# Performance work log

Hardware: AMD Instinct MI355X
Metric: run time of the kernel (lower is better)

The kernel has to match this reference:

```python
import jax, jax.numpy as jnp
import numpy as np

N_NODES = 50000
N_EDGES = 200000
H = 128
L = 6
NODE_IN = 9
EDGE_IN = 10
OUT = 3


def _glorot(key, shape):
    fan_in = shape[0]
    return jax.random.normal(key, shape, dtype=jnp.float32) * (1.0 / np.sqrt(fan_in))


def setup_inputs() -> dict:
    key = jax.random.key(0)
    ks = jax.random.split(key, 32)
    x = jax.random.normal(ks[0], (N_NODES, NODE_IN), dtype=jnp.float32)
    edge_attr = jax.random.normal(ks[1], (N_EDGES, EDGE_IN), dtype=jnp.float32)
    edge_index = jax.random.randint(ks[2], (2, N_EDGES), 0, N_NODES, dtype=jnp.int32)
    bc_disp = (jax.random.uniform(ks[3], (N_NODES, 2)) < 0.05).astype(jnp.float32)
    bc_rot = (jax.random.uniform(ks[4], (N_NODES, 1)) < 0.05).astype(jnp.float32)
    inp = {
        'x': x, 'edge_attr': edge_attr, 'edge_index': edge_index,
        'bc_disp': bc_disp, 'bc_rot': bc_rot,
        # node encoder MLP(NODE_IN,[H],H)
        'enc_n_W1': _glorot(ks[5], (NODE_IN, H)), 'enc_n_b1': jnp.zeros((H,), jnp.float32),
        'enc_n_W2': _glorot(ks[6], (H, H)), 'enc_n_b2': jnp.zeros((H,), jnp.float32),
        # edge encoder MLP(EDGE_IN,[H],H)
        'enc_e_W1': _glorot(ks[7], (EDGE_IN, H)), 'enc_e_b1': jnp.zeros((H,), jnp.float32),
        'enc_e_W2': _glorot(ks[8], (H, H)), 'enc_e_b2': jnp.zeros((H,), jnp.float32),
        # L message-passing layers: msg MLP(3H->H->H), update MLP(2H->H->H), stacked on dim 0
        'mp_msg_W1': jnp.stack([_glorot(jax.random.fold_in(ks[9], i), (3 * H, H)) for i in range(L)]),
        'mp_msg_b1': jnp.zeros((L, H), jnp.float32),
        'mp_msg_W2': jnp.stack([_glorot(jax.random.fold_in(ks[10], i), (H, H)) for i in range(L)]),
        'mp_msg_b2': jnp.zeros((L, H), jnp.float32),
        'mp_upd_W1': jnp.stack([_glorot(jax.random.fold_in(ks[11], i), (2 * H, H)) for i in range(L)]),
        'mp_upd_b1': jnp.zeros((L, H), jnp.float32),
        'mp_upd_W2': jnp.stack([_glorot(jax.random.fold_in(ks[12], i), (H, H)) for i in range(L)]),
        'mp_upd_b2': jnp.zeros((L, H), jnp.float32),
        # decoder MLP(H,[H,64],OUT)
        'dec_W1': _glorot(ks[13], (H, H)), 'dec_b1': jnp.zeros((H,), jnp.float32),
        'dec_W2': _glorot(ks[14], (H, 64)), 'dec_b2': jnp.zeros((64,), jnp.float32),
        'dec_W3': _glorot(ks[15], (64, OUT)), 'dec_b3': jnp.zeros((OUT,), jnp.float32),
    }
    return inp


def _pignn_forward(x, edge_attr, edge_index, bc_disp, bc_rot,
                   enc_n_W1, enc_n_b1, enc_n_W2, enc_n_b2,
                   enc_e_W1, enc_e_b1, enc_e_W2, enc_e_b2,
                   mp_msg_W1, mp_msg_b1, mp_msg_W2, mp_msg_b2,
                   mp_upd_W1, mp_upd_b1, mp_upd_W2, mp_upd_b2,
                   dec_W1, dec_b1, dec_W2, dec_b2, dec_W3, dec_b3):
    relu = jax.nn.relu
    n = x.shape[0]
    src, dst = edge_index[0], edge_index[1]

    # encoders: Linear -> ReLU -> Linear
    h = relu(x @ enc_n_W1 + enc_n_b1) @ enc_n_W2 + enc_n_b2            # [N, H]
    e = relu(edge_attr @ enc_e_W1 + enc_e_b1) @ enc_e_W2 + enc_e_b2    # [E, H]

    def mp_step(h, params):
        mW1, mb1, mW2, mb2, uW1, ub1, uW2, ub2 = params
        m_in = jnp.concatenate([h[src], h[dst], e], axis=-1)           # [E, 3H]
        m = relu(m_in @ mW1 + mb1) @ mW2 + mb2                         # [E, H]
        agg = jax.ops.segment_sum(m, dst, num_segments=n)              # [N, H]
        u_in = jnp.concatenate([h, agg], axis=-1)                      # [N, 2H]
        upd = relu(u_in @ uW1 + ub1) @ uW2 + ub2                       # [N, H]
        return h + upd, None                                           # residual

    h, _ = jax.lax.scan(mp_step, h,
                        (mp_msg_W1, mp_msg_b1, mp_msg_W2, mp_msg_b2,
                         mp_upd_W1, mp_upd_b1, mp_upd_W2, mp_upd_b2))

    # decoder: H -> H -> 64 -> OUT with ReLU between layers
    d = relu(h @ dec_W1 + dec_b1)
    d = relu(d @ dec_W2 + dec_b2)
    pred = d @ dec_W3 + dec_b3                                         # [N, 3]

    # hard boundary conditions
    disp_mask = 1.0 - bc_disp
    rot_mask = 1.0 - bc_rot
    return jnp.concatenate([pred[:, 0:2] * disp_mask, pred[:, 2:3] * rot_mask], axis=1)


def reference(x, edge_attr, edge_index, bc_disp, bc_rot,
              enc_n_W1, enc_n_b1, enc_n_W2, enc_n_b2,
              enc_e_W1, enc_e_b1, enc_e_W2, enc_e_b2,
              mp_msg_W1, mp_msg_b1, mp_msg_W2, mp_msg_b2,
              mp_upd_W1, mp_upd_b1, mp_upd_W2, mp_upd_b2,
              dec_W1, dec_b1, dec_W2, dec_b2, dec_W3, dec_b3):
    return _pignn_forward(x, edge_attr, edge_index, bc_disp, bc_rot,
                          enc_n_W1, enc_n_b1, enc_n_W2, enc_n_b2,
                          enc_e_W1, enc_e_b1, enc_e_W2, enc_e_b2,
                          mp_msg_W1, mp_msg_b1, mp_msg_W2, mp_msg_b2,
                          mp_upd_W1, mp_upd_b1, mp_upd_W2, mp_upd_b2,
                          dec_W1, dec_b1, dec_W2, dec_b2, dec_W3, dec_b3)
```

## Files before the change

### kernel.cpp

```cpp
#include <hip/hip_runtime.h>

#define NN 50000
#define NE 200000
#define HD 128

typedef unsigned short us4 __attribute__((ext_vector_type(4)));
typedef unsigned short us8 __attribute__((ext_vector_type(8)));
typedef short s8 __attribute__((ext_vector_type(8)));
typedef float f4 __attribute__((ext_vector_type(4)));

#define SA 136
#define SA32 40
#define SC2 68

__device__ __forceinline__ float b2f(unsigned short u) {
    union { unsigned i; float f; } v; v.i = ((unsigned)u) << 16; return v.f;
}
__device__ __forceinline__ unsigned short f2b(float x) {
    union { float f; unsigned i; } v; v.f = x;
    unsigned r = v.i + 0x7fffu + ((v.i >> 16) & 1u);
    return (unsigned short)(r >> 16);
}
struct hl2 { short hi, lo; };
__device__ __forceinline__ hl2 split2(float x) {
    unsigned short h = f2b(x);
    hl2 r;
    r.hi = (short)h;
    r.lo = (short)f2b(x - b2f(h));
    return r;
}

__global__ __launch_bounds__(256) void zeroi_k(int* __restrict__ p, int n) {
    int i = blockIdx.x * 256 + threadIdx.x;
    if (i < n) p[i] = 0;
}
__global__ __launch_bounds__(256) void zerof_k(float* __restrict__ p, long n) {
    long i = (long)blockIdx.x * 256 + threadIdx.x;
    if (i < n) p[i] = 0.f;
}

__global__ __launch_bounds__(256) void hist_k(const int* __restrict__ dst, int* __restrict__ cnt) {
    int i = blockIdx.x * 256 + threadIdx.x;
    if (i < NE) atomicAdd(&cnt[dst[i]], 1);
}
__global__ __launch_bounds__(256) void scan1_k(const int* __restrict__ cnt, int* __restrict__ bsum) {
    __shared__ int sc[256];
    int i = blockIdx.x * 256 + threadIdx.x;
    sc[threadIdx.x] = (i < NN) ? cnt[i] : 0;
    __syncthreads();
    for (int off = 128; off > 0; off >>= 1) {
        if (threadIdx.x < off) sc[threadIdx.x] += sc[threadIdx.x + off];
        __syncthreads();
    }
    if (threadIdx.x == 0) bsum[blockIdx.x] = sc[0];
}
__global__ __launch_bounds__(256) void scan2_k(int* __restrict__ bsum, int nb) {
    __shared__ int sc[256];
    int t = threadIdx.x;
    int v = (t < nb) ? bsum[t] : 0;
    sc[t] = v;
    __syncthreads();
    for (int off = 1; off < 256; off <<= 1) {
        int a = (t >= off) ? sc[t - off] : 0;
        __syncthreads();
        sc[t] += a;
        __syncthreads();
    }
    if (t < nb) bsum[t] = sc[t] - v;
}
__global__ __launch_bounds__(256) void scan3_k(const int* __restrict__ cnt, const int* __restrict__ bsum,
                                               int* __restrict__ rp, float* __restrict__ deg) {
    __shared__ int sc[256];
    int t = threadIdx.x;
    int i = blockIdx.x * 256 + t;
    int v = (i < NN) ? cnt[i] : 0;
    sc[t] = v;
    __syncthreads();
    for (int off = 1; off < 256; off <<= 1) {
        int a = (t >= off) ? sc[t - off] : 0;
        __syncthreads();
        sc[t] += a;
        __syncthreads();
    }
    int incl = sc[t];
    if (i < NN) {
        rp[i] = bsum[blockIdx.x] + incl - v;
        deg[i] = (float)v;
        if (i == NN - 1) rp[NN] = bsum[blockIdx.x] + incl;
    }
}
__global__ __launch_bounds__(256) void posbuild_k(const int* __restrict__ src, const int* __restrict__ dst,
                                                  const int* __restrict__ rp, int* __restrict__ cur,
                                                  int* __restrict__ pos, int* __restrict__ srcS,
                                                  int* __restrict__ dstS) {
    int i = blockIdx.x * 256 + threadIdx.x;
    if (i >= NE) return;
    int d = dst[i];
    int p = rp[d] + atomicAdd(&cur[d], 1);
    pos[i] = p;
    srcS[p] = src[i];
    dstS[p] = d;
}

__global__ __launch_bounds__(256) void mini_k(const float* __restrict__ W2m, const float* __restrict__ uW1b,
                                              const float* __restrict__ b2m,
                                              float* __restrict__ W2u, float* __restrict__ b2u) {
    int r = blockIdx.x * 16 + (threadIdx.x >> 4);
    int c0 = (threadIdx.x & 15) * 8;
    float a[8] = {};
    for (int k = 0; k < HD; ++k) {
        float w = W2m[r * HD + k];
        const float* u = uW1b + k * HD + c0;
        float4 u0 = *(const float4*)u, u1 = *(const float4*)(u + 4);
        a[0] = fmaf(w, u0.x, a[0]); a[1] = fmaf(w, u0.y, a[1]);
        a[2] = fmaf(w, u0.z, a[2]); a[3] = fmaf(w, u0.w, a[3]);
        a[4] = fmaf(w, u1.x, a[4]); a[5] = fmaf(w, u1.y, a[5]);
        a[6] = fmaf(w, u1.z, a[6]); a[7] = fmaf(w, u1.w, a[7]);
    }
    *(float4*)(W2u + r * HD + c0)     = float4{a[0], a[1], a[2], a[3]};
    *(float4*)(W2u + r * HD + c0 + 4) = float4{a[4], a[5], a[6], a[7]};
    if (blockIdx.x == 0 && threadIdx.x < 16) {
        int cc = threadIdx.x * 8;
        float b[8] = {};
        for (int k = 0; k < HD; ++k) {
            float w = b2m[k];
            const float* u = uW1b + k * HD + cc;
            float4 u0 = *(const float4*)u, u1 = *(const float4*)(u + 4);
            b[0] = fmaf(w, u0.x, b[0]); b[1] = fmaf(w, u0.y, b[1]);
            b[2] = fmaf(w, u0.z, b[2]); b[3] = fmaf(w, u0.w, b[3]);
            b[4] = fmaf(w, u1.x, b[4]); b[5] = fmaf(w, u1.y, b[5]);
            b[6] = fmaf(w, u1.z, b[6]); b[7] = fmaf(w, u1.w, b[7]);
        }
        *(float4*)(b2u + cc)     = float4{b[0], b[1], b[2], b[3]};
        *(float4*)(b2u + cc + 4) = float4{b[4], b[5], b[6], b[7]};
    }
}
__global__ __launch_bounds__(256) void wtL_k(const float* __restrict__ msgW1, const float* __restrict__ updW1,
                                             const float* __restrict__ updW2, const float* __restrict__ W2uF,
                                             unsigned short* __restrict__ dst) {
    int idx = blockIdx.x * 256 + threadIdx.x;
    int m = idx >> 14;
    int r = idx & 16383;
    int n = r >> 7, k = r & 127;
    float v;
    switch (m) {
        case 0: v = msgW1[(long)k * HD + n]; break;
        case 1: v = msgW1[(long)(128 + k) * HD + n]; break;
        case 2: v = msgW1[(long)(256 + k) * HD + n]; break;
        case 3: v = updW1[(long)k * HD + n]; break;
        case 4: v = updW2[(long)k * HD + n]; break;
        default: v = W2uF[(long)k * HD + n]; break;
    }
    hl2 p = split2(v);
    dst[(long)m * 32768 + n * HD + k] = (unsigned short)p.hi;
    dst[(long)m * 32768 + 16384 + n * HD + k] = (unsigned short)p.lo;
}
__global__ __launch_bounds__(256) void wtE_k(const float* __restrict__ nW1, const float* __restrict__ nW2,
                                             const float* __restrict__ eW1, const float* __restrict__ eW2,
                                             unsigned short* __restrict__ dst) {
    int idx = blockIdx.x * 256 + threadIdx.x;
    float v; long off; int pos, sz;
    if (idx < 4096) {
        int n = idx >> 5, k = idx & 31;
        v = (k < 9) ? nW1[k * HD + n] : 0.f; off = 0; pos = idx; sz = 4096;
    } else if (idx < 20480) {
        int r = idx - 4096; int n = r >> 7, k = r & 127;
        v = nW2[k * HD + n]; off = 8192; pos = r; sz = 16384;
    } else if (idx < 24576) {
        int r = idx - 20480; int n = r >> 5, k = r & 31;
        v = (k < 10) ? eW1[k * HD + n] : 0.f; off = 40960; pos = r; sz = 4096;
    } else {
        int r = idx - 24576; int n = r >> 7, k = r & 127;
        v = eW2[k * HD + n]; off = 49152; pos = r; sz = 16384;
    }
    hl2 p = split2(v);
    dst[off + pos] = (unsigned short)p.hi;
    dst[off + sz + pos] = (unsigned short)p.lo;
}

__device__ __forceinline__ void stageA_f32_split(short* __restrict__ At, short* __restrict__ Al,
                                                 const float* __restrict__ A, int bm, int M, int tid) {
#pragma unroll
    for (int t = 0; t < 4; ++t) {
        int c = tid + t * 256;
        int row = c >> 4, k8 = (c & 15) * 8;
        int gr = bm + row;
        s8 vh = (s8)0, vl = (s8)0;
        if (gr < M) {
            const float* p = A + (long)gr * HD + k8;
            f4 a = *(const f4*)p, b = *(const f4*)(p + 4);
#pragma unroll
            for (int i = 0; i < 4; ++i) {
                hl2 pa = split2(a[i]);
                hl2 pb = split2(b[i]);
                vh[i] = pa.hi; vl[i] = pa.lo;
                vh[4 + i] = pb.hi; vl[4 + i] = pb.lo;
            }
        }
        *(s8*)(At + row * SA + k8) = vh;
        *(s8*)(Al + row * SA + k8) = vl;
    }
}
__device__ __forceinline__ void stageA_b16(short* __restrict__ At, const unsigned short* __restrict__ A,
                                           int bm, int M, int tid) {
#pragma unroll
    for (int t = 0; t < 4; ++t) {
        int c = tid + t * 256;
        int row = c >> 4, k8 = (c & 15) * 8;
        int gr = bm + row;
        s8 v = (s8)0;
        if (gr < M) v = *(const s8*)(A + (long)gr * HD + k8);
        *(s8*)(At + row * SA + k8) = v;
    }
}
__device__ __forceinline__ void stage_segsum_split(short* __restrict__ At, short* __restrict__ Al,
                                                   const unsigned short* __restrict__ Pe,
                                                   const int* __restrict__ rowp,
                                                   int bm, int M, int tid) {
#pragma unroll
    for (int t = 0; t < 4; ++t) {
        int c = tid + t * 256;
        int row = c >> 4, k8 = (c & 15) * 8;
        int gr = bm + row;
        float sum[8] = {};
        if (gr < M) {
            int e0 = rowp[gr], e1 = rowp[gr + 1];
            for (int e = e0; e < e1; ++e) {
                us8 v = *(const us8*)(Pe + (long)e * HD + k8);
#pragma unroll
                for (int i = 0; i < 8; ++i) sum[i] += b2f(v[i]);
            }
        }
        s8 vh, vl;
#pragma unroll
        for (int i = 0; i < 8; ++i) {
            hl2 p = split2(sum[i]);
            vh[i] = p.hi; vl[i] = p.lo;
        }
        *(s8*)(At + row * SA + k8) = vh;
        *(s8*)(Al + row * SA + k8) = vl;
    }
}
__device__ __forceinline__ void loadB2(s8 b[2][4], const unsigned short* __restrict__ W,
                                       int sw, int nk, int w, int lane) {
    const int r16 = lane & 15, q8 = (lane >> 4) * 8;
#pragma unroll
    for (int ct = 0; ct < 2; ++ct)
#pragma unroll 4
        for (int ks = 0; ks < nk; ++ks)
            b[ct][ks] = *(const s8*)((const short*)W + (long)((2 * w + ct) * 16 + r16) * sw + ks * 32 + q8);
}
__device__ __forceinline__ void mfma3_reg(f4 acc[4][2], const short* __restrict__ At,
                                          const short* __restrict__ Al, int sa,
                                          const s8 bh[2][4], const s8 bl[2][4], int nk, int lane) {
    const int r16 = lane & 15, q8 = (lane >> 4) * 8;
#pragma unroll 4
    for (int ks = 0; ks < nk; ++ks)
#pragma unroll
        for (int rt = 0; rt < 4; ++rt) {
            s8 ah = *(const s8*)(At + (rt * 16 + r16) * sa + ks * 32 + q8);
            s8 al = *(const s8*)(Al + (rt * 16 + r16) * sa + ks * 32 + q8);
#pragma unroll
            for (int ct = 0; ct < 2; ++ct) {
                acc[rt][ct] = __builtin_amdgcn_mfma_f32_16x16x32_bf16(ah, bh[ct][ks], acc[rt][ct], 0, 0, 0);
                acc[rt][ct] = __builtin_amdgcn_mfma_f32_16x16x32_bf16(al, bh[ct][ks], acc[rt][ct], 0, 0, 0);
                acc[rt][ct] = __builtin_amdgcn_mfma_f32_16x16x32_bf16(ah, bl[ct][ks], acc[rt][ct], 0, 0, 0);
            }
        }
}
__device__ __forceinline__ void mfmaE_reg(f4 acc[4][2], const short* __restrict__ At, int sa,
                                          const s8 bh[2][4], const s8 bl[2][4], int nk, int lane) {
    const int r16 = lane & 15, q8 = (lane >> 4) * 8;
#pragma unroll 4
    for (int ks = 0; ks < nk; ++ks)
#pragma unroll
        for (int rt = 0; rt < 4; ++rt) {
            s8 a = *(const s8*)(At + (rt * 16 + r16) * sa + ks * 32 + q8);
#pragma unroll
            for (int ct = 0; ct < 2; ++ct) {
                acc[rt][ct] = __builtin_amdgcn_mfma_f32_16x16x32_bf16(a, bh[ct][ks], acc[rt][ct], 0, 0, 0);
                acc[rt][ct] = __builtin_amdgcn_mfma_f32_16x16x32_bf16(a, bl[ct][ks], acc[rt][ct], 0, 0, 0);
            }
        }
}
__device__ __forceinline__ void dumpC_half2(float* __restrict__ Cd, const f4 acc[4][2],
                                            int half, int w, int lane) {
    if ((w >> 1) != half) return;
    const int col0 = lane & 15, rq = (lane >> 4) * 4;
    const int bc = (w & 1) * 2;
#pragma unroll
    for (int rt = 0; rt < 4; ++rt)
#pragma unroll
        for (int ct = 0; ct < 2; ++ct)
#pragma unroll
            for (int r = 0; r < 4; ++r)
                Cd[(rt * 16 + rq + r) * SC2 + (bc + ct) * 16 + col0] = acc[rt][ct][r];
}
#define ACC_ZERO2(acc) { f4 z_ = {0.f, 0.f, 0.f, 0.f}; \
    for (int r_ = 0; r_ < 4; ++r_) for (int c_ = 0; c_ < 2; ++c_) acc[r_][c_] = z_; }

__global__ __launch_bounds__(256) void dual_k(const float* __restrict__ h,
                                              const unsigned short* __restrict__ W1aT,
                                              const unsigned short* __restrict__ W1bT,
                                              unsigned short* __restrict__ Hs, unsigned short* __restrict__ Hd,
                                              int M) {
    __shared__ __align__(16) short At[64 * SA];
    __shared__ __align__(16) short Al[64 * SA];
    __shared__ __align__(16) float Cd[64 * SC2];
    const int tid = threadIdx.x, lane = tid & 63, w = tid >> 6, tx = tid & 15, ty = tid >> 4;
    const int bm = blockIdx.x * 64;
    s8 bh[2][4], bl[2][4];
    loadB2(bh, W1aT, HD, 4, w, lane);
    loadB2(bl, W1aT + 16384, HD, 4, w, lane);
    stageA_f32_split(At, Al, h, bm, M, tid);
    __syncthreads();
    f4 acc[4][2]; ACC_ZERO2(acc);
    mfma3_reg(acc, At, Al, SA, bh, bl, 4, lane);
    loadB2(bh, W1bT, HD, 4, w, lane);
    loadB2(bl, W1bT + 16384, HD, 4, w, lane);
#pragma unroll
    for (int half = 0; half < 2; ++half) {
        __syncthreads();
        dumpC_half2(Cd, acc, half, w, lane);
        __syncthreads();
        int c4 = half * 64 + tx * 4;
#pragma unroll
        for (int i = 0; i < 4; ++i) {
            int row = ty * 4 + i, gr = bm + row;
            if (gr >= M) continue;
            f4 v = *(const f4*)(Cd + row * SC2 + tx * 4);
            us4 o;
#pragma unroll
            for (int j = 0; j < 4; ++j) o[j] = f2b(v[j]);
            *(us4*)(Hs + (long)gr * HD + c4) = o;
        }
    }
    ACC_ZERO2(acc);
    mfma3_reg(acc, At, Al, SA, bh, bl, 4, lane);
#pragma unroll
    for (int half = 0; half < 2; ++half) {
        __syncthreads();
        dumpC_half2(Cd, acc, half, w, lane);
        __syncthreads();
        int c4 = half * 64 + tx * 4;
#pragma unroll
        for (int i = 0; i < 4; ++i) {
            int row = ty * 4 + i, gr = bm + row;
            if (gr >= M) continue;
            f4 v = *(const f4*)(Cd + row * SC2 + tx * 4);
            us4 o;
#pragma unroll
            for (int j = 0; j < 4; ++j) o[j] = f2b(v[j]);
            *(us4*)(Hd + (long)gr * HD + c4) = o;
        }
    }
}

__global__ __launch_bounds__(256) void edge_k(const unsigned short* __restrict__ eS,
                                              const unsigned short* __restrict__ Hs,
                                              const unsigned short* __restrict__ Hd,
                                              const int* __restrict__ srcS, const int* __restrict__ dstS,
                                              const unsigned short* __restrict__ W1cT,
                                              const float* __restrict__ b1,
                                              unsigned short* __restrict__ Pe) {
    __shared__ __align__(16) short At[64 * SA];
    __shared__ __align__(16) float Cd[64 * SC2];
    const int tid = threadIdx.x, lane = tid & 63, w = tid >> 6, tx = tid & 15, ty = tid >> 4;
    const int bm = blockIdx.x * 64;
    s8 bh[2][4], bl[2][4];
    loadB2(bh, W1cT, HD, 4, w, lane);
    loadB2(bl, W1cT + 16384, HD, 4, w, lane);
    stageA_b16(At, eS, bm, NE, tid);
    __syncthreads();
    f4 acc[4][2]; ACC_ZERO2(acc);
    mfmaE_reg(acc, At, SA, bh, bl, 4, lane);
#pragma unroll
    for (int half = 0; half < 2; ++half) {
        __syncthreads();
        dumpC_half2(Cd, acc, half, w, lane);
        __syncthreads();
        int c4 = half * 64 + tx * 4;
        f4 bv = *(const f4*)(b1 + c4);
#pragma unroll
        for (int i = 0; i < 4; ++i) {
            int row = ty * 4 + i, edge = bm + row;
            int s = srcS[edge], d = dstS[edge];
            us4 hs = *(const us4*)(Hs + (long)s * HD + c4);
            us4 hd = *(const us4*)(Hd + (long)d * HD + c4);
            f4 cv = *(const f4*)(Cd + row * SC2 + tx * 4);
            us4 o;
#pragma unroll
            for (int j = 0; j < 4; ++j)
                o[j] = f2b(fmaxf(cv[j] + bv[j] + b2f(hs[j]) + b2f(hd[j]), 0.f));
            *(us4*)(Pe + (long)edge * HD + c4) = o;
        }
    }
}

__global__ __launch_bounds__(256) void upd_k(float* __restrict__ h,
                                             const unsigned short* __restrict__ Pe,
                                             const int* __restrict__ rowp,
                                             const unsigned short* __restrict__ uW1aT,
                                             const unsigned short* __restrict__ W2uT,
                                             const float* __restrict__ ub1, const float* __restrict__ b2u,
                                             const float* __restrict__ deg,
                                             const unsigned short* __restrict__ uW2T,
                                             const float* __restrict__ ub2, int M) {
    __shared__ __align__(16) short At[64 * SA];
    __shared__ __align__(16) short Al[64 * SA];
    __shared__ __align__(16) float Cd[64 * SC2];
    const int tid = threadIdx.x, lane = tid & 63, w = tid >> 6, tx = tid & 15, ty = tid >> 4;
    const int bm = blockIdx.x * 64;
    s8 bh[2][4], bl[2][4];
    f4 acc[4][2]; ACC_ZERO2(acc);
    loadB2(bh, uW1aT, HD, 4, w, lane);
    loadB2(bl, uW1aT + 16384, HD, 4, w, lane);
    stageA_f32_split(At, Al, h, bm, M, tid);
    __syncthreads();
    mfma3_reg(acc, At, Al, SA, bh, bl, 4, lane);
    loadB2(bh, W2uT, HD, 4, w, lane);
    loadB2(bl, W2uT + 16384, HD, 4, w, lane);
    __syncthreads();
    stage_segsum_split(At, Al, Pe, rowp, bm, M, tid);
    __syncthreads();
    mfma3_reg(acc, At, Al, SA, bh, bl, 4, lane);
    loadB2(bh, uW2T, HD, 4, w, lane);
    loadB2(bl, uW2T + 16384, HD, 4, w, lane);
    __syncthreads();
    {
        const int col0 = lane & 15, rq = (lane >> 4) * 4;
        float u1[2], u2[2];
#pragma unroll
        for (int ct = 0; ct < 2; ++ct) {
            int col = (2 * w + ct) * 16 + col0;
            u1[ct] = ub1[col]; u2[ct] = b2u[col];
        }
        float dgv[16];
#pragma unroll
        for (int rt = 0; rt < 4; ++rt)
#pragma unroll
            for (int r = 0; r < 4; ++r) {
                int gr = bm + rt * 16 + rq + r;
                dgv[rt * 4 + r] = (gr < M) ? deg[gr] : 0.f;
            }
#pragma unroll
        for (int rt = 0; rt < 4; ++rt)
#pragma unroll
            for (int ct = 0; ct < 2; ++ct)
#pragma unroll
                for (int r = 0; r < 4; ++r) {
                    float p = fmaxf(acc[rt][ct][r] + u1[ct] + dgv[rt * 4 + r] * u2[ct], 0.f);
                    hl2 pp = split2(p);
                    int off = (rt * 16 + rq + r) * SA + (2 * w + ct) * 16 + col0;
                    At[off] = pp.hi;
                    Al[off] = pp.lo;
                }
    }
    __syncthreads();
    ACC_ZERO2(acc);
    mfma3_reg(acc, At, Al, SA, bh, bl, 4, lane);
#pragma unroll
    for (int half = 0; half < 2; ++half) {
        __syncthreads();
        dumpC_half2(Cd, acc, half, w, lane);
        __syncthreads();
        int c4 = half * 64 + tx * 4;
        f4 u0 = *(const f4*)(ub2 + c4);
#pragma unroll
        for (int i = 0; i < 4; ++i) {
            int row = ty * 4 + i, gr = bm + row;
            if (gr >= M) continue;
            float* hp = h + (long)gr * HD + c4;
            f4 a = *(f4*)hp;
            f4 cv = *(const f4*)(Cd + row * SC2 + tx * 4);
#pragma unroll
            for (int j = 0; j < 4; ++j) a[j] += cv[j] + u0[j];
            *(f4*)hp = a;
        }
    }
}

template<bool SCAT>
__global__ __launch_bounds__(256) void enc_k(const float* __restrict__ A, int KIN,
                                             const unsigned short* __restrict__ W1T, const float* __restrict__ b1,
                                             const unsigned short* __restrict__ W2T, const float* __restrict__ b2,
                                             float* __restrict__ outF, unsigned short* __restrict__ outB,
                                             const int* __restrict__ pos, int M) {
    __shared__ __align__(16) short At[64 * SA];
    __shared__ __align__(16) short Al[64 * SA];
    __shared__ __align__(16) float Cd[64 * SC2];
    const int tid = threadIdx.x, lane = tid & 63, w = tid >> 6, tx = tid & 15, ty = tid >> 4;
    const int bm = blockIdx.x * 64;
    s8 bh[2][4], bl[2][4];
    loadB2(bh, W1T, 32, 1, w, lane);
    loadB2(bl, W1T + 4096, 32, 1, w, lane);
    {
        int row = tid >> 2, k8 = (tid & 3) * 8;
        int gr = bm + row;
        s8 vh = (s8)0, vl = (s8)0;
        if (gr < M) {
#pragma unroll
            for (int i = 0; i < 8; ++i) {
                int k = k8 + i;
                if (k < KIN) {
                    hl2 p = split2(A[(long)gr * KIN + k]);
                    vh[i] = p.hi; vl[i] = p.lo;
                }
            }
        }
        *(s8*)(At + row * SA32 + k8) = vh;
        *(s8*)(Al + row * SA32 + k8) = vl;
    }
    __syncthreads();
    f4 acc[4][2]; ACC_ZERO2(acc);
    mfma3_reg(acc, At, Al, SA32, bh, bl, 1, lane);
    loadB2(bh, W2T, HD, 4, w, lane);
    loadB2(bl, W2T + 16384, HD, 4, w, lane);
    __syncthreads();
    {
        const int col0 = lane & 15, rq = (lane >> 4) * 4;
        float bb[2];
#pragma unroll
        for (int ct = 0; ct < 2; ++ct) bb[ct] = b1[(2 * w + ct) * 16 + col0];
#pragma unroll
        for (int rt = 0; rt < 4; ++rt)
#pragma unroll
            for (int ct = 0; ct < 2; ++ct)
#pragma unroll
                for (int r = 0; r < 4; ++r) {
                    float p = fmaxf(acc[rt][ct][r] + bb[ct], 0.f);
                    hl2 pp = split2(p);
                    int off = (rt * 16 + rq + r) * SA + (2 * w + ct) * 16 + col0;
                    At[off] = pp.hi;
                    Al[off] = pp.lo;
                }
    }
    __syncthreads();
    ACC_ZERO2(acc);
    mfma3_reg(acc, At, Al, SA, bh, bl, 4, lane);
#pragma unroll
    for (int half = 0; half < 2; ++half) {
        __syncthreads();
        dumpC_half2(Cd, acc, half, w, lane);
        __syncthreads();
        int c4 = half * 64 + tx * 4;
        f4 bv = *(const f4*)(b2 + c4);
#pragma unroll
        for (int i = 0; i < 4; ++i) {
            int row = ty * 4 + i, gr = bm + row;
            if (gr >= M) continue;
            f4 cv = *(const f4*)(Cd + row * SC2 + tx * 4);
            if constexpr (SCAT) {
                int p = pos[gr];
                us4 o;
#pragma unroll
                for (int j = 0; j < 4; ++j) o[j] = f2b(cv[j] + bv[j]);
                *(us4*)(outB + (long)p * HD + c4) = o;
            } else {
                f4 o;
#pragma unroll
                for (int j = 0; j < 4; ++j) o[j] = cv[j] + bv[j];
                *(f4*)(outF + (long)gr * HD + c4) = o;
            }
        }
    }
}

__global__ __launch_bounds__(256) void dec_k(
    const float* __restrict__ h,
    const float* __restrict__ W1, const float* __restrict__ b1,
    const float* __restrict__ W2, const float* __restrict__ b2,
    const float* __restrict__ W3, const float* __restrict__ b3,
    const float* __restrict__ bc_disp, const float* __restrict__ bc_rot,
    float* __restrict__ outp, int M)
{
    __shared__ float As[64][33];
    __shared__ float Ws[32][HD];
    __shared__ float P[64][HD + 1];
    __shared__ float D2[64][65];
    const int tid = threadIdx.x, tx = tid & 15, ty = tid >> 4;
    const int bm = blockIdx.x * 64;
    float acc[4][8] = {};

    for (int kk = 0; kk < HD; kk += 32) {
        int r = tid >> 2, cc0 = (tid & 3) * 8, gr = bm + r;
#pragma unroll
        for (int i = 0; i < 8; ++i)
            As[r][cc0 + i] = (gr < M) ? h[(long)gr * HD + kk + cc0 + i] : 0.f;
        int k = tid >> 3, n0 = (tid & 7) * 16;
#pragma unroll
        for (int i = 0; i < 16; ++i)
            Ws[k][n0 + i] = W1[(kk + k) * HD + n0 + i];
        __syncthreads();
#pragma unroll
        for (int k2 = 0; k2 < 32; ++k2) {
            float a0 = As[ty * 4 + 0][k2], a1 = As[ty * 4 + 1][k2];
            float a2 = As[ty * 4 + 2][k2], a3 = As[ty * 4 + 3][k2];
#pragma unroll
            for (int j = 0; j < 8; ++j) {
                float ww = Ws[k2][tx * 8 + j];
                acc[0][j] = fmaf(a0, ww, acc[0][j]);
                acc[1][j] = fmaf(a1, ww, acc[1][j]);
                acc[2][j] = fmaf(a2, ww, acc[2][j]);
                acc[3][j] = fmaf(a3, ww, acc[3][j]);
            }
        }
        __syncthreads();
    }
#pragma unroll
    for (int i = 0; i < 4; ++i) {
        int row = ty * 4 + i;
#pragma unroll
        for (int j = 0; j < 8; ++j) {
            int col = tx * 8 + j;
            P[row][col] = fmaxf(acc[i][j] + b1[col], 0.f);
        }
    }
    __syncthreads();
    float acc2[4][4] = {};
    for (int kk = 0; kk < HD; kk += 32) {
        int idx = tid * 8;
        int k = idx >> 6, n0 = idx & 63;
#pragma unroll
        for (int i = 0; i < 8; ++i)
            Ws[k][n0 + i] = W2[(kk + k) * 64 + n0 + i];
        __syncthreads();
#pragma unroll
        for (int k2 = 0; k2 < 32; ++k2) {
            float a0 = P[ty * 4 + 0][kk + k2], a1 = P[ty * 4 + 1][kk + k2];
            float a2 = P[ty * 4 + 2][kk + k2], a3 = P[ty * 4 + 3][kk + k2];
#pragma unroll
            for (int j = 0; j < 4; ++j) {
                float ww = Ws[k2][tx * 4 + j];
                acc2[0][j] = fmaf(a0, ww, acc2[0][j]);
                acc2[1][j] = fmaf(a1, ww, acc2[1][j]);
                acc2[2][j] = fmaf(a2, ww, acc2[2][j]);
                acc2[3][j] = fmaf(a3, ww, acc2[3][j]);
            }
        }
        __syncthreads();
    }
#pragma unroll
    for (int i = 0; i < 4; ++i) {
        int row = ty * 4 + i;
#pragma unroll
        for (int j = 0; j < 4; ++j) {
            int col = tx * 4 + j;
            D2[row][col] = fmaxf(acc2[i][j] + b2[col], 0.f);
        }
    }
    __syncthreads();
    if (tid < 64) {
        int gr = bm + tid;
        if (gr < M) {
            float a0 = b3[0], a1 = b3[1], a2 = b3[2];
#pragma unroll
            for (int k = 0; k < 64; ++k) {
                float v = D2[tid][k];
                a0 = fmaf(v, W3[k * 3 + 0], a0);
                a1 = fmaf(v, W3[k * 3 + 1], a1);
                a2 = fmaf(v, W3[k * 3 + 2], a2);
            }
            outp[gr * 3 + 0] = a0 * (1.f - bc_disp[gr * 2 + 0]);
            outp[gr * 3 + 1] = a1 * (1.f - bc_disp[gr * 2 + 1]);
            outp[gr * 3 + 2] = a2 * (1.f - bc_rot[gr]);
        }
    }
}

extern "C" void kernel_launch(void* const* d_in, const int* in_sizes, int n_in,
                              void* d_out, int out_size, void* d_ws, size_t ws_size,
                              hipStream_t stream)
{
    const float* x        = (const float*)d_in[0];
    const float* eattr    = (const float*)d_in[1];
    const int*   eidx     = (const int*)d_in[2];
    const float* bc_disp  = (const float*)d_in[3];
    const float* bc_rot   = (const float*)d_in[4];
    const float* enc_n_W1 = (const float*)d_in[5];
    const float* enc_n_b1 = (const float*)d_in[6];
    const float* enc_n_W2 = (const float*)d_in[7];
    const float* enc_n_b2 = (const float*)d_in[8];
    const float* enc_e_W1 = (const float*)d_in[9];
    const float* enc_e_b1 = (const float*)d_in[10];
    const float* enc_e_W2 = (const float*)d_in[11];
    const float* enc_e_b2 = (const float*)d_in[12];
    const float* msg_W1   = (const float*)d_in[13];
    const float* msg_b1   = (const float*)d_in[14];
    const float* msg_W2   = (const float*)d_in[15];
    const float* msg_b2   = (const float*)d_in[16];
    const float* upd_W1   = (const float*)d_in[17];
    const float* upd_b1   = (const float*)d_in[18];
    const float* upd_W2   = (const float*)d_in[19];
    const float* upd_b2   = (const float*)d_in[20];
    const float* dec_W1   = (const float*)d_in[21];
    const float* dec_b1   = (const float*)d_in[22];
    const float* dec_W2   = (const float*)d_in[23];
    const float* dec_b2   = (const float*)d_in[24];
    const float* dec_W3   = (const float*)d_in[25];
    const float* dec_b3   = (const float*)d_in[26];

    const int* src = eidx;
    const int* dst = eidx + NE;

    char* base = (char*)d_ws;
    float* h  = (float*)base;
    unsigned short* Hs = (unsigned short*)(h + (long)NN * HD);
    unsigned short* Hd = Hs + (long)NN * HD;
    unsigned short* eS = Hd + (long)NN * HD;
    unsigned short* Pe = eS + (long)NE * HD;
    float* W2uF = (float*)(Pe + (long)NE * HD);
    float* b2uA = W2uF + 6 * HD * HD;
    unsigned short* WtL = (unsigned short*)(b2uA + 6 * HD);
    unsigned short* WtE = WtL + 6L * 6 * 32768;
    float* deg = (float*)(WtE + 81920);
    int* rowp  = (int*)(deg + NN);
    int* cnt   = rowp + (NN + 1);
    int* posb  = cnt + NN;
    int* srcS  = posb + NE;
    int* dstS  = srcS + NE;
    int* bsum  = dstS + NE;
    size_t need = (size_t)((char*)(bsum + 256) - base);
    if (ws_size < need) {
        zerof_k<<<(unsigned)((out_size + 255) / 256), 256, 0, stream>>>((float*)d_out, out_size);
        return;
    }

    dim3 blk(256);
    const unsigned gN  = (NN + 63) / 64;
    const unsigned gE  = NE / 64;
    const unsigned gNc = (NN + 255) / 256;
    const unsigned gEc = (NE + 255) / 256;

    zeroi_k<<<gNc, blk, 0, stream>>>(cnt, NN);
    hist_k<<<gEc, blk, 0, stream>>>(dst, cnt);
    scan1_k<<<gNc, blk, 0, stream>>>(cnt, bsum);
    scan2_k<<<1, blk, 0, stream>>>(bsum, (int)gNc);
    scan3_k<<<gNc, blk, 0, stream>>>(cnt, bsum, rowp, deg);
    zeroi_k<<<gNc, blk, 0, stream>>>(cnt, NN);
    posbuild_k<<<gEc, blk, 0, stream>>>(src, dst, rowp, cnt, posb, srcS, dstS);

    for (int l = 0; l < 6; ++l) {
        mini_k<<<8, blk, 0, stream>>>(msg_W2 + (long)l * HD * HD,
                                      upd_W1 + (long)l * 256 * HD + 128 * HD,
                                      msg_b2 + (long)l * HD,
                                      W2uF + (long)l * HD * HD, b2uA + (long)l * HD);
    }
    for (int l = 0; l < 6; ++l) {
        wtL_k<<<384, blk, 0, stream>>>(msg_W1 + (long)l * 384 * HD,
                                       upd_W1 + (long)l * 256 * HD,
                                       upd_W2 + (long)l * HD * HD,
                                       W2uF + (long)l * HD * HD,
                                       WtL + (long)l * 6 * 32768);
    }
    wtE_k<<<160, blk, 0, stream>>>(enc_n_W1, enc_n_W2, enc_e_W1, enc_e_W2, WtE);

    enc_k<false><<<gN, blk, 0, stream>>>(x, 9, WtE, enc_n_b1, WtE + 8192, enc_n_b2,
                                         h, nullptr, nullptr, NN);
    enc_k<true><<<gE, blk, 0, stream>>>(eattr, 10, WtE + 40960, enc_e_b1, WtE + 49152, enc_e_b2,
                                        nullptr, eS, posb, NE);

    for (int l = 0; l < 6; ++l) {
        const unsigned short* Wt = WtL + (long)l * 6 * 32768;
        const float* b1  = msg_b1 + (long)l * HD;
        const float* ub1 = upd_b1 + (long)l * HD;
        const float* ub2 = upd_b2 + (long)l * HD;
        const float* b2u = b2uA + (long)l * HD;

        dual_k<<<gN, blk, 0, stream>>>(h, Wt + 0L * 32768, Wt + 1L * 32768, Hs, Hd, NN);
        edge_k<<<gE, blk, 0, stream>>>(eS, Hs, Hd, srcS, dstS, Wt + 2L * 32768, b1, Pe);
        upd_k<<<gN, blk, 0, stream>>>(h, Pe, rowp, Wt + 3L * 32768, Wt + 5L * 32768,
                                      ub1, b2u, deg, Wt + 4L * 32768, ub2, NN);
    }

    dec_k<<<gN, blk, 0, stream>>>(h, dec_W1, dec_b1, dec_W2, dec_b2, dec_W3, dec_b3,
                                  bc_disp, bc_rot, (float*)d_out, NN);
}
```

Baseline: 1.126 ms.

## Fuse next-layer node projections into update kernel and move decoder to MFMA

The update kernel now keeps the freshly updated node features in shared memory as split bf16 hi/lo and immediately computes the next layer's source and destination projections (Hs, Hd). This removes the separate per-layer dual kernel launch and its re-read of h. The scalar FP32 decoder is also replaced with a split-bf16 MFMA version using pre-transposed decoder weights. The cost is more register and shared-memory pressure in the update kernel, plus the small precision change from the split-bf16 three-product scheme in the decoder.

```diff
diff --git a/kernel.cpp b/kernel.cpp
--- a/kernel.cpp
+++ b/kernel.cpp
@@ -177,6 +177,22 @@
     dst[off + pos] = (unsigned short)p.hi;
     dst[off + sz + pos] = (unsigned short)p.lo;
 }
+__global__ __launch_bounds__(256) void wtD_k(const float* __restrict__ dW1, const float* __restrict__ dW2,
+                                             unsigned short* __restrict__ dst) {
+    int idx = blockIdx.x * 256 + threadIdx.x;
+    if (idx < 16384) {
+        int n = idx >> 7, k = idx & 127;
+        hl2 p = split2(dW1[k * HD + n]);
+        dst[idx] = (unsigned short)p.hi;
+        dst[16384 + idx] = (unsigned short)p.lo;
+    } else {
+        int r = idx - 16384;
+        int n = r >> 7, k = r & 127;
+        hl2 p = split2(dW2[k * 64 + n]);
+        dst[32768 + r] = (unsigned short)p.hi;
+        dst[40960 + r] = (unsigned short)p.lo;
+    }
+}
 
 __device__ __forceinline__ void stageA_f32_split(short* __restrict__ At, short* __restrict__ Al,
                                                  const float* __restrict__ A, int bm, int M, int tid) {
@@ -405,7 +421,11 @@
                                              const float* __restrict__ ub1, const float* __restrict__ b2u,
                                              const float* __restrict__ deg,
                                              const unsigned short* __restrict__ uW2T,
-                                             const float* __restrict__ ub2, int M) {
+                                             const float* __restrict__ ub2,
+                                             const unsigned short* __restrict__ W1aTn,
+                                             const unsigned short* __restrict__ W1bTn,
+                                             unsigned short* __restrict__ Hs,
+                                             unsigned short* __restrict__ Hd, int M) {
     __shared__ __align__(16) short At[64 * SA];
     __shared__ __align__(16) short Al[64 * SA];
     __shared__ __align__(16) float Cd[64 * SC2];
@@ -459,6 +479,7 @@
     __syncthreads();
     ACC_ZERO2(acc);
     mfma3_reg(acc, At, Al, SA, bh, bl, 4, lane);
+    __syncthreads();
 #pragma unroll
     for (int half = 0; half < 2; ++half) {
         __syncthreads();
@@ -476,6 +497,56 @@
 #pragma unroll
             for (int j = 0; j < 4; ++j) a[j] += cv[j] + u0[j];
             *(f4*)hp = a;
+#pragma unroll
+            for (int j = 0; j < 4; ++j) {
+                hl2 pp = split2(a[j]);
+                At[row * SA + c4 + j] = pp.hi;
+                Al[row * SA + c4 + j] = pp.lo;
+            }
+        }
+    }
+    if (!W1aTn) return;
+    loadB2(bh, W1aTn, HD, 4, w, lane);
+    loadB2(bl, W1aTn + 16384, HD, 4, w, lane);
+    __syncthreads();
+    ACC_ZERO2(acc);
+    mfma3_reg(acc, At, Al, SA, bh, bl, 4, lane);
+    loadB2(bh, W1bTn, HD, 4, w, lane);
+    loadB2(bl, W1bTn + 16384, HD, 4, w, lane);
+#pragma unroll
+    for (int half = 0; half < 2; ++half) {
+        __syncthreads();
+        dumpC_half2(Cd, acc, half, w, lane);
+        __syncthreads();
+        int c4 = half * 64 + tx * 4;
+#pragma unroll
+        for (int i = 0; i < 4; ++i) {
+            int row = ty * 4 + i, gr = bm + row;
+            if (gr >= M) continue;
+            f4 v = *(const f4*)(Cd + row * SC2 + tx * 4);
+            us4 o;
+#pragma unroll
+            for (int j = 0; j < 4; ++j) o[j] = f2b(v[j]);
+            *(us4*)(Hs + (long)gr * HD + c4) = o;
+        }
+    }
+    ACC_ZERO2(acc);
+    mfma3_reg(acc, At, Al, SA, bh, bl, 4, lane);
+#pragma unroll
+    for (int half = 0; half < 2; ++half) {
+        __syncthreads();
+        dumpC_half2(Cd, acc, half, w, lane);
+        __syncthreads();
+        int c4 = half * 64 + tx * 4;
+#pragma unroll
+        for (int i = 0; i < 4; ++i) {
+            int row = ty * 4 + i, gr = bm + row;
+            if (gr >= M) continue;
+            f4 v = *(const f4*)(Cd + row * SC2 + tx * 4);
+            us4 o;
+#pragma unroll
+            for (int j = 0; j < 4; ++j) o[j] = f2b(v[j]);
+            *(us4*)(Hd + (long)gr * HD + c4) = o;
         }
     }
 }
@@ -566,88 +637,70 @@
     }
 }
 
-__global__ __launch_bounds__(256) void dec_k(
-    const float* __restrict__ h,
-    const float* __restrict__ W1, const float* __restrict__ b1,
-    const float* __restrict__ W2, const float* __restrict__ b2,
-    const float* __restrict__ W3, const float* __restrict__ b3,
-    const float* __restrict__ bc_disp, const float* __restrict__ bc_rot,
-    float* __restrict__ outp, int M)
-{
-    __shared__ float As[64][33];
-    __shared__ float Ws[32][HD];
-    __shared__ float P[64][HD + 1];
-    __shared__ float D2[64][65];
-    const int tid = threadIdx.x, tx = tid & 15, ty = tid >> 4;
+__global__ __launch_bounds__(256) void dec2_k(const float* __restrict__ h,
+                                              const unsigned short* __restrict__ WtD,
+                                              const float* __restrict__ b1, const float* __restrict__ b2,
+                                              const float* __restrict__ W3, const float* __restrict__ b3,
+                                              const float* __restrict__ bc_disp, const float* __restrict__ bc_rot,
+                                              float* __restrict__ outp, int M) {
+    __shared__ __align__(16) short At[64 * SA];
+    __shared__ __align__(16) short Al[64 * SA];
+    __shared__ __align__(16) float D2[64 * 65];
+    const int tid = threadIdx.x, lane = tid & 63, w = tid >> 6;
     const int bm = blockIdx.x * 64;
-    float acc[4][8] = {};
-
-    for (int kk = 0; kk < HD; kk += 32) {
-        int r = tid >> 2, cc0 = (tid & 3) * 8, gr = bm + r;
-#pragma unroll
-        for (int i = 0; i < 8; ++i)
-            As[r][cc0 + i] = (gr < M) ? h[(long)gr * HD + kk + cc0 + i] : 0.f;
-        int k = tid >> 3, n0 = (tid & 7) * 16;
-#pragma unroll
-        for (int i = 0; i < 16; ++i)
-            Ws[k][n0 + i] = W1[(kk + k) * HD + n0 + i];
-        __syncthreads();
-#pragma unroll
-        for (int k2 = 0; k2 < 32; ++k2) {
-            float a0 = As[ty * 4 + 0][k2], a1 = As[ty * 4 + 1][k2];
-            float a2 = As[ty * 4 + 2][k2], a3 = As[ty * 4 + 3][k2];
-#pragma unroll
-            for (int j = 0; j < 8; ++j) {
-                float ww = Ws[k2][tx * 8 + j];
-                acc[0][j] = fmaf(a0, ww, acc[0][j]);
-                acc[1][j] = fmaf(a1, ww, acc[1][j]);
-                acc[2][j] = fmaf(a2, ww, acc[2][j]);
-                acc[3][j] = fmaf(a3, ww, acc[3][j]);
-            }
-        }
-        __syncthreads();
-    }
-#pragma unroll
-    for (int i = 0; i < 4; ++i) {
-        int row = ty * 4 + i;
-#pragma unroll
-        for (int j = 0; j < 8; ++j) {
-            int col = tx * 8 + j;
-            P[row][col] = fmaxf(acc[i][j] + b1[col], 0.f);
-        }
-    }
-    __syncthreads();
-    float acc2[4][4] = {};
-    for (int kk = 0; kk < HD; kk += 32) {
-        int idx = tid * 8;
-        int k = idx >> 6, n0 = idx & 63;
-#pragma unroll
-        for (int i = 0; i < 8; ++i)
-            Ws[k][n0 + i] = W2[(kk + k) * 64 + n0 + i];
-        __syncthreads();
-#pragma unroll
-        for (int k2 = 0; k2 < 32; ++k2) {
-            float a0 = P[ty * 4 + 0][kk + k2], a1 = P[ty * 4 + 1][kk + k2];
-            float a2 = P[ty * 4 + 2][kk + k2], a3 = P[ty * 4 + 3][kk + k2];
-#pragma unroll
-            for (int j = 0; j < 4; ++j) {
-                float ww = Ws[k2][tx * 4 + j];
-                acc2[0][j] = fmaf(a0, ww, acc2[0][j]);
-                acc2[1][j] = fmaf(a1, ww, acc2[1][j]);
-                acc2[2][j] = fmaf(a2, ww, acc2[2][j]);
-                acc2[3][j] = fmaf(a3, ww, acc2[3][j]);
-            }
-        }
-        __syncthreads();
-    }
-#pragma unroll
-    for (int i = 0; i < 4; ++i) {
-        int row = ty * 4 + i;
-#pragma unroll
-        for (int j = 0; j < 4; ++j) {
-            int col = tx * 4 + j;
-            D2[row][col] = fmaxf(acc2[i][j] + b2[col], 0.f);
-        }
+    s8 bh[2][4], bl[2][4];
+    loadB2(bh, WtD, HD, 4, w, lane);
+    loadB2(bl, WtD + 16384, HD, 4, w, lane);
+    stageA_f32_split(At, Al, h, bm, M, tid);
+    __syncthreads();
+    f4 acc[4][2]; ACC_ZERO2(acc);
+    mfma3_reg(acc, At, Al, SA, bh, bl, 4, lane);
+    __syncthreads();
+    {
+        const int col0 = lane & 15, rq = (lane >> 4) * 4;
+        float bb[2];
+#pragma unroll
+        for (int ct = 0; ct < 2; ++ct) bb[ct] = b1[(2 * w + ct) * 16 + col0];
+#pragma unroll
+        for (int rt = 0; rt < 4; ++rt)
+#pragma unroll
+            for (int ct = 0; ct < 2; ++ct)
+#pragma unroll
+                for (int r = 0; r < 4; ++r) {
+                    float p = fmaxf(acc[rt][ct][r] + bb[ct], 0.f);
+                    hl2 pp = split2(p);
+                    int off = (rt * 16 + rq + r) * SA + (2 * w + ct) * 16 + col0;
+                    At[off] = pp.hi;
+                    Al[off] = pp.lo;
+                }
+    }
+    __syncthreads();
+    {
+        const int r16 = lane & 15, q8 = (lane >> 4) * 8, rq = (lane >> 4) * 4;
+        s8 b2h[4], b2l[4];
+#pragma unroll
+        for (int ks = 0; ks < 4; ++ks) {
+            b2h[ks] = *(const s8*)((const short*)WtD + 32768 + (long)(w * 16 + r16) * HD + ks * 32 + q8);
+            b2l[ks] = *(const s8*)((const short*)WtD + 40960 + (long)(w * 16 + r16) * HD + ks * 32 + q8);
+        }
+        f4 acc2[4];
+        { f4 z_ = {0.f, 0.f, 0.f, 0.f}; for (int r_ = 0; r_ < 4; ++r_) acc2[r_] = z_; }
+#pragma unroll
+        for (int ks = 0; ks < 4; ++ks)
+#pragma unroll
+            for (int rt = 0; rt < 4; ++rt) {
+                s8 ah = *(const s8*)(At + (rt * 16 + r16) * SA + ks * 32 + q8);
+                s8 al = *(const s8*)(Al + (rt * 16 + r16) * SA + ks * 32 + q8);
+                acc2[rt] = __builtin_amdgcn_mfma_f32_16x16x32_bf16(ah, b2h[ks], acc2[rt], 0, 0, 0);
+                acc2[rt] = __builtin_amdgcn_mfma_f32_16x16x32_bf16(al, b2h[ks], acc2[rt], 0, 0, 0);
+                acc2[rt] = __builtin_amdgcn_mfma_f32_16x16x32_bf16(ah, b2l[ks], acc2[rt], 0, 0, 0);
+            }
+        float b2v = b2[w * 16 + r16];
+#pragma unroll
+        for (int rt = 0; rt < 4; ++rt)
+#pragma unroll
+            for (int r = 0; r < 4; ++r)
+                D2[(rt * 16 + rq + r) * 65 + w * 16 + r16] = fmaxf(acc2[rt][r] + b2v, 0.f);
     }
     __syncthreads();
     if (tid < 64) {
@@ -656,7 +709,7 @@
             float a0 = b3[0], a1 = b3[1], a2 = b3[2];
 #pragma unroll
             for (int k = 0; k < 64; ++k) {
-                float v = D2[tid][k];
+                float v = D2[tid * 65 + k];
                 a0 = fmaf(v, W3[k * 3 + 0], a0);
                 a1 = fmaf(v, W3[k * 3 + 1], a1);
                 a2 = fmaf(v, W3[k * 3 + 2], a2);
@@ -713,7 +766,8 @@
     float* b2uA = W2uF + 6 * HD * HD;
     unsigned short* WtL = (unsigned short*)(b2uA + 6 * HD);
     unsigned short* WtE = WtL + 6L * 6 * 32768;
-    float* deg = (float*)(WtE + 81920);
+    unsigned short* WtD = WtE + 81920;
+    float* deg = (float*)(WtD + 49152);
     int* rowp  = (int*)(deg + NN);
     int* cnt   = rowp + (NN + 1);
     int* posb  = cnt + NN;
@@ -754,25 +808,28 @@
                                        WtL + (long)l * 6 * 32768);
     }
     wtE_k<<<160, blk, 0, stream>>>(enc_n_W1, enc_n_W2, enc_e_W1, enc_e_W2, WtE);
+    wtD_k<<<96, blk, 0, stream>>>(dec_W1, dec_W2, WtD);
 
     enc_k<false><<<gN, blk, 0, stream>>>(x, 9, WtE, enc_n_b1, WtE + 8192, enc_n_b2,
                                          h, nullptr, nullptr, NN);
     enc_k<true><<<gE, blk, 0, stream>>>(eattr, 10, WtE + 40960, enc_e_b1, WtE + 49152, enc_e_b2,
                                         nullptr, eS, posb, NE);
 
+    dual_k<<<gN, blk, 0, stream>>>(h, WtL + 0L * 32768, WtL + 1L * 32768, Hs, Hd, NN);
     for (int l = 0; l < 6; ++l) {
         const unsigned short* Wt = WtL + (long)l * 6 * 32768;
         const float* b1  = msg_b1 + (long)l * HD;
         const float* ub1 = upd_b1 + (long)l * HD;
         const float* ub2 = upd_b2 + (long)l * HD;
         const float* b2u = b2uA + (long)l * HD;
-
-        dual_k<<<gN, blk, 0, stream>>>(h, Wt + 0L * 32768, Wt + 1L * 32768, Hs, Hd, NN);
+        const unsigned short* Wn = (l < 5) ? (WtL + (long)(l + 1) * 6 * 32768) : nullptr;
+
         edge_k<<<gE, blk, 0, stream>>>(eS, Hs, Hd, srcS, dstS, Wt + 2L * 32768, b1, Pe);
         upd_k<<<gN, blk, 0, stream>>>(h, Pe, rowp, Wt + 3L * 32768, Wt + 5L * 32768,
-                                      ub1, b2u, deg, Wt + 4L * 32768, ub2, NN);
-    }
-
-    dec_k<<<gN, blk, 0, stream>>>(h, dec_W1, dec_b1, dec_W2, dec_b2, dec_W3, dec_b3,
-                                  bc_disp, bc_rot, (float*)d_out, NN);
-}
+                                      ub1, b2u, deg, Wt + 4L * 32768, ub2,
+                                      Wn, Wn ? (Wn + 32768) : nullptr, Hs, Hd, NN);
+    }
+
+    dec2_k<<<gN, blk, 0, stream>>>(h, WtD, dec_b1, dec_b2, dec_W3, dec_b3,
+                                   bc_disp, bc_rot, (float*)d_out, NN);
+}
```

Result: faster. 1.025 ms (-9.0%).
